# Kernel tuning notes

Measured on AMD Instinct MI355X. Metric: run time of the kernel, lower is better.

## Reference

```python
import jax, jax.numpy as jnp
import numpy as np

B, N, W, D = 32, 576, 32, 256  # batch, patches, max concepts per sample, embed dim


def _l2norm(x, eps=1e-12):
    # matches torch F.normalize: x / max(||x||, eps)
    n = jnp.linalg.norm(x, axis=-1, keepdims=True)
    return x / jnp.maximum(n, eps)


def setup_inputs() -> dict:
    key = jax.random.key(0)
    k1, k2, k3 = jax.random.split(key, 3)
    return {
        "image_token_features": jax.random.normal(k1, (B, N, D), dtype=jnp.float32),
        "concept_text_features": jax.random.normal(k2, (B, W, D), dtype=jnp.float32),
        "concept_lengths": jax.random.randint(k3, (B,), 1, W + 1, dtype=jnp.int32),
        "logit_scale": jnp.array([2.0], dtype=jnp.float32),   # log-scale, clamp(-10,10).exp()
        "logit_bias": jnp.array([-1.0], dtype=jnp.float32),
    }


def reference(image_token_features, concept_text_features, logit_scale, logit_bias, concept_lengths):
    img = _l2norm(image_token_features)          # (B, N, D)
    con = _l2norm(concept_text_features)         # (B, W, D)
    # A[m, c, n, w] = cos(patch_n of image m, concept_w of sample c)
    A = jnp.einsum('mnd,cwd->mcnw', img, con)    # (B, B, N, W) -- dominant intermediate
    max_per_concept = A.max(axis=2)              # max over patches -> (B, B, W)
    # masked mean over valid concepts (ragged lengths)
    mask = (jnp.arange(W)[None, :] < concept_lengths[:, None]).astype(img.dtype)  # (B, W)
    lens = concept_lengths.astype(img.dtype)     # all >= 1 by construction
    sim = jnp.sum(max_per_concept * mask[None, :, :], axis=-1) / lens[None, :]    # (B, B)
    t = jnp.exp(jnp.clip(logit_scale, -10.0, 10.0))[0]
    logits = jnp.clip(t * sim + logit_bias[0], -50.0, 50.0)
    z = 2.0 * jnp.eye(sim.shape[0], dtype=sim.dtype) - 1.0  # +1 diag, -1 off-diag
    loss = -jnp.mean(jax.nn.log_sigmoid(z * logits))
    return loss
```

## Files before the change

### kernel.cpp

```cpp
#include <hip/hip_runtime.h>
#include <hip/hip_bf16.h>
#include <math.h>

#define BB 32
#define NP 576
#define WW 32
#define DD 256

typedef __bf16 bf16x8 __attribute__((ext_vector_type(8)));
typedef float f32x4 __attribute__((ext_vector_type(4)));

__device__ __forceinline__ unsigned short f2bf(float f) {
  unsigned int u = __float_as_uint(f);
  u += 0x7FFFu + ((u >> 16) & 1u);
  return (unsigned short)(u >> 16);
}

__device__ __forceinline__ void gld_lds16(const unsigned short* g, unsigned short* l) {
  __builtin_amdgcn_global_load_lds(
      (const __attribute__((address_space(1))) void*)g,
      (__attribute__((address_space(3))) void*)l, 16, 0, 0);
}

__device__ __forceinline__ unsigned int encf(float f) {
  unsigned int b = __float_as_uint(f);
  return (b & 0x80000000u) ? ~b : (b | 0x80000000u);
}
__device__ __forceinline__ float decf(unsigned int u) {
  unsigned int b = (u & 0x80000000u) ? (u & 0x7FFFFFFFu) : ~u;
  return __uint_as_float(b);
}

__global__ __launch_bounds__(256) void norm_cast_kernel(
    const float* __restrict__ img, const float* __restrict__ con,
    unsigned short* __restrict__ img_t, unsigned short* __restrict__ con_t,
    unsigned int* __restrict__ sraw) {
  int gid = blockIdx.x * 256 + threadIdx.x;
  if (gid < BB * 1024) sraw[gid] = 0u;

  int row = blockIdx.x * 4 + (threadIdx.x >> 6);
  int lane = threadIdx.x & 63;
  const int n_img = BB * NP;
  const float* src;
  unsigned short* dstbase;
  int prow;
  if (row < n_img) {
    src = img + (size_t)row * DD;
    dstbase = img_t;
    prow = row;
  } else {
    prow = row - n_img;
    src = con + (size_t)prow * DD;
    dstbase = con_t;
  }
  float4 v = ((const float4*)src)[lane];
  float ss = v.x * v.x + v.y * v.y + v.z * v.z + v.w * v.w;
  #pragma unroll
  for (int off = 1; off < 64; off <<= 1) ss += __shfl_xor(ss, off);
  float inv = 1.0f / fmaxf(sqrtf(ss), 1e-12f);
  ushort4 o;
  o.x = f2bf(v.x * inv);
  o.y = f2bf(v.y * inv);
  o.z = f2bf(v.z * inv);
  o.w = f2bf(v.w * inv);
  size_t di = ((size_t)(prow >> 4) * 8 + (lane >> 3)) * 512 +
              (size_t)((((lane >> 1) & 3) * 16 + (prow & 15)) * 8) + (lane & 1) * 4;
  *(ushort4*)(dstbase + di) = o;
}

__global__ __launch_bounds__(256, 3) void gemm_max_kernel(
    const unsigned short* __restrict__ img_t,
    const unsigned short* __restrict__ con_t,
    unsigned int* __restrict__ sraw) {
  int bx = blockIdx.x;
  int bw = bx & 7;
  int bm = bx >> 3;
  int m = bm / 5;
  int t = bm - m * 5;
  int p0 = m * NP + t * 128;
  int w0 = bw * 128;

  __shared__ __align__(16) unsigned short ldsA[8192];
  __shared__ float sm[256];

  int tid = threadIdx.x;
  int wid = tid >> 6;
  int lane = tid & 63;
  int wp = wid >> 1;
  int wc = wid & 1;

  f32x4 acc[4][4];
  #pragma unroll
  for (int i = 0; i < 4; ++i)
    #pragma unroll
    for (int j = 0; j < 4; ++j) acc[i][j] = (f32x4){0.f, 0.f, 0.f, 0.f};

  const unsigned short* gA = img_t + (size_t)(p0 >> 4) * 4096 + lane * 8;
  const unsigned short* gB = con_t + ((size_t)(w0 >> 4) + wc * 4) * 4096 + lane * 8;

  for (int kb = 0; kb < 4; ++kb) {
    __syncthreads();
    #pragma unroll
    for (int u = 0; u < 4; ++u) {
      int s = wid * 4 + u;
      int gi = s >> 1;
      int kk2 = s & 1;
      gld_lds16(gA + ((size_t)gi * 8 + kb * 2 + kk2) * 512, &ldsA[s * 512]);
    }
    bf16x8 bfr[4][2];
    #pragma unroll
    for (int wj = 0; wj < 4; ++wj)
      #pragma unroll
      for (int kk = 0; kk < 2; ++kk)
        bfr[wj][kk] =
            *(const bf16x8*)(gB + ((size_t)wj * 8 + kb * 2 + kk) * 512);
    __syncthreads();
    #pragma unroll
    for (int kk = 0; kk < 2; ++kk) {
      bf16x8 af[4];
      #pragma unroll
      for (int pi = 0; pi < 4; ++pi)
        af[pi] = *(const bf16x8*)&ldsA[(((wp * 4 + pi) << 1) | kk) * 512 + lane * 8];
      #pragma unroll
      for (int pi = 0; pi < 4; ++pi)
        #pragma unroll
        for (int wj = 0; wj < 4; ++wj)
          acc[pi][wj] = __builtin_amdgcn_mfma_f32_16x16x32_bf16(
              af[pi], bfr[wj][kk], acc[pi][wj], 0, 0, 0);
    }
  }

  float mxw[4];
  #pragma unroll
  for (int wj = 0; wj < 4; ++wj) {
    float v = -1e30f;
    #pragma unroll
    for (int pi = 0; pi < 4; ++pi)
      v = fmaxf(v, fmaxf(fmaxf(acc[pi][wj][0], acc[pi][wj][1]),
                         fmaxf(acc[pi][wj][2], acc[pi][wj][3])));
    v = fmaxf(v, __shfl_xor(v, 16));
    v = fmaxf(v, __shfl_xor(v, 32));
    mxw[wj] = v;
  }
  __syncthreads();
  if (lane < 16) {
    #pragma unroll
    for (int wj = 0; wj < 4; ++wj)
      sm[wp * 128 + wc * 64 + wj * 16 + lane] = mxw[wj];
  }
  __syncthreads();
  if (tid < 128) {
    float v = sm[tid];
    if (t != 4) v = fmaxf(v, sm[128 + tid]);
    atomicMax(&sraw[(size_t)m * 1024 + w0 + tid], encf(v));
  }
}

__global__ __launch_bounds__(1024) void loss_kernel(
    const unsigned int* __restrict__ sraw, const int* __restrict__ lens,
    const float* __restrict__ lsc, const float* __restrict__ lbi,
    float* __restrict__ out) {
  int tid = threadIdx.x;
  int m = tid >> 5;
  int c = tid & 31;
  int len = lens[c];
  const unsigned int* base = sraw + (size_t)m * 1024 + c * 32;
  float s = 0.0f;
  for (int w = 0; w < WW; ++w)
    if (w < len) s += decf(base[w]);
  s /= (float)len;
  float tt = expf(fminf(fmaxf(lsc[0], -10.0f), 10.0f));
  float lg = fminf(fmaxf(tt * s + lbi[0], -50.0f), 50.0f);
  float x = (m == c) ? lg : -lg;
  float acc = (x >= 0.0f) ? -log1pf(expf(-x)) : (x - log1pf(expf(x)));
  #pragma unroll
  for (int off = 1; off < 64; off <<= 1) acc += __shfl_xor(acc, off);
  __shared__ float sred[16];
  if ((tid & 63) == 0) sred[tid >> 6] = acc;
  __syncthreads();
  if (tid == 0) {
    float tot = 0.0f;
    #pragma unroll
    for (int i = 0; i < 16; ++i) tot += sred[i];
    out[0] = -tot / (float)(BB * BB);
  }
}

extern "C" void kernel_launch(void* const* d_in, const int* in_sizes, int n_in,
                              void* d_out, int out_size, void* d_ws, size_t ws_size,
                              hipStream_t stream) {
  const float* img = (const float*)d_in[0];
  const float* con = (const float*)d_in[1];
  const int* lens = (const int*)d_in[2];
  const float* lsc = (const float*)d_in[3];
  const float* lbi = (const float*)d_in[4];

  unsigned short* img_t = (unsigned short*)d_ws;
  unsigned short* con_t = img_t + (size_t)BB * NP * DD;
  unsigned int* sraw = (unsigned int*)(con_t + (size_t)BB * WW * DD);

  norm_cast_kernel<<<(BB * NP + BB * WW) / 4, 256, 0, stream>>>(img, con, img_t,
                                                                con_t, sraw);
  gemm_max_kernel<<<160 * 8, 256, 0, stream>>>(img_t, con_t, sraw);
  loss_kernel<<<1, 1024, 0, stream>>>(sraw, lens, lsc, lbi, (float*)d_out);
}
```

Before: 102.5 us.

## Stage B tiles through LDS, coalesce norm-cast writes, remap blocks for XCD locality

The norm/cast kernel now handles 16 rows per 1024-thread block and stages the bf16 output in LDS. It then writes each 4096-element tile contiguously instead of scattering 8-byte stores. The GEMM kernel now loads concept (B) tiles into LDS with global_load_lds rather than per-wave direct global loads. Block indices are also remapped so that blocks sharing an image tile land on the same XCD for L2 reuse. The cost is extra LDS use in the GEMM, which may reduce occupancy, plus an extra barrier in the cast kernel.

```diff
diff --git a/kernel.cpp b/kernel.cpp
--- a/kernel.cpp
+++ b/kernel.cpp
@@ -31,29 +31,31 @@
   return __uint_as_float(b);
 }
 
-__global__ __launch_bounds__(256) void norm_cast_kernel(
+__global__ __launch_bounds__(1024) void norm_cast_kernel(
     const float* __restrict__ img, const float* __restrict__ con,
     unsigned short* __restrict__ img_t, unsigned short* __restrict__ con_t,
     unsigned int* __restrict__ sraw) {
-  int gid = blockIdx.x * 256 + threadIdx.x;
-  if (gid < BB * 1024) sraw[gid] = 0u;
-
-  int row = blockIdx.x * 4 + (threadIdx.x >> 6);
-  int lane = threadIdx.x & 63;
-  const int n_img = BB * NP;
+  __shared__ __align__(16) unsigned short lds[16 * 264];
+  int tid = threadIdx.x;
+  int g = blockIdx.x;
+  if (g < 32) sraw[g * 1024 + tid] = 0u;
+
+  int w = tid >> 6;
+  int L = tid & 63;
+  const int n_img_g = (BB * NP) >> 4;
   const float* src;
   unsigned short* dstbase;
-  int prow;
-  if (row < n_img) {
-    src = img + (size_t)row * DD;
+  int gl;
+  if (g < n_img_g) {
+    src = img + ((size_t)g * 16 + w) * DD;
     dstbase = img_t;
-    prow = row;
+    gl = g;
   } else {
-    prow = row - n_img;
-    src = con + (size_t)prow * DD;
+    gl = g - n_img_g;
+    src = con + ((size_t)gl * 16 + w) * DD;
     dstbase = con_t;
   }
-  float4 v = ((const float4*)src)[lane];
+  float4 v = ((const float4*)src)[L];
   float ss = v.x * v.x + v.y * v.y + v.z * v.z + v.w * v.w;
   #pragma unroll
   for (int off = 1; off < 64; off <<= 1) ss += __shfl_xor(ss, off);
@@ -63,9 +65,17 @@
   o.y = f2bf(v.y * inv);
   o.z = f2bf(v.z * inv);
   o.w = f2bf(v.w * inv);
-  size_t di = ((size_t)(prow >> 4) * 8 + (lane >> 3)) * 512 +
-              (size_t)((((lane >> 1) & 3) * 16 + (prow & 15)) * 8) + (lane & 1) * 4;
-  *(ushort4*)(dstbase + di) = o;
+  *(ushort4*)&lds[w * 264 + L * 4] = o;
+  __syncthreads();
+  int i = tid * 4;
+  int s = i >> 9;
+  int idx8 = (i & 511) >> 3;
+  int q = idx8 >> 4;
+  int r = idx8 & 15;
+  int ji = i & 7;
+  int k = (s >> 1) * 64 + (s & 1) * 32 + q * 8 + ji;
+  ushort4 val = *(const ushort4*)&lds[r * 264 + k];
+  *(ushort4*)(dstbase + (size_t)gl * 4096 + i) = val;
 }
 
 __global__ __launch_bounds__(256, 3) void gemm_max_kernel(
@@ -73,14 +83,17 @@
     const unsigned short* __restrict__ con_t,
     unsigned int* __restrict__ sraw) {
   int bx = blockIdx.x;
-  int bw = bx & 7;
-  int bm = bx >> 3;
+  int xcd = bx & 7;
+  int k2 = bx >> 3;
+  int bm = (k2 & ~7) | xcd;
+  int bw = k2 & 7;
   int m = bm / 5;
   int t = bm - m * 5;
   int p0 = m * NP + t * 128;
   int w0 = bw * 128;
 
   __shared__ __align__(16) unsigned short ldsA[8192];
+  __shared__ __align__(16) unsigned short ldsB[8192];
   __shared__ float sm[256];
 
   int tid = threadIdx.x;
@@ -96,7 +109,7 @@
     for (int j = 0; j < 4; ++j) acc[i][j] = (f32x4){0.f, 0.f, 0.f, 0.f};
 
   const unsigned short* gA = img_t + (size_t)(p0 >> 4) * 4096 + lane * 8;
-  const unsigned short* gB = con_t + ((size_t)(w0 >> 4) + wc * 4) * 4096 + lane * 8;
+  const unsigned short* gB = con_t + (size_t)(w0 >> 4) * 4096 + lane * 8;
 
   for (int kb = 0; kb < 4; ++kb) {
     __syncthreads();
@@ -105,28 +118,26 @@
       int s = wid * 4 + u;
       int gi = s >> 1;
       int kk2 = s & 1;
-      gld_lds16(gA + ((size_t)gi * 8 + kb * 2 + kk2) * 512, &ldsA[s * 512]);
+      size_t goff = ((size_t)gi * 8 + kb * 2 + kk2) * 512;
+      gld_lds16(gA + goff, &ldsA[s * 512]);
+      gld_lds16(gB + goff, &ldsB[s * 512]);
     }
-    bf16x8 bfr[4][2];
-    #pragma unroll
-    for (int wj = 0; wj < 4; ++wj)
-      #pragma unroll
-      for (int kk = 0; kk < 2; ++kk)
-        bfr[wj][kk] =
-            *(const bf16x8*)(gB + ((size_t)wj * 8 + kb * 2 + kk) * 512);
     __syncthreads();
     #pragma unroll
     for (int kk = 0; kk < 2; ++kk) {
-      bf16x8 af[4];
+      bf16x8 af[4], bfr[4];
       #pragma unroll
       for (int pi = 0; pi < 4; ++pi)
         af[pi] = *(const bf16x8*)&ldsA[(((wp * 4 + pi) << 1) | kk) * 512 + lane * 8];
       #pragma unroll
+      for (int wj = 0; wj < 4; ++wj)
+        bfr[wj] = *(const bf16x8*)&ldsB[(((wc * 4 + wj) << 1) | kk) * 512 + lane * 8];
+      #pragma unroll
       for (int pi = 0; pi < 4; ++pi)
         #pragma unroll
         for (int wj = 0; wj < 4; ++wj)
-          acc[pi][wj] = __builtin_amdgcn_mfma_f32_16x16x32_bf16(
-              af[pi], bfr[wj][kk], acc[pi][wj], 0, 0, 0);
+          acc[pi][wj] = __builtin_amdgcn_mfma_f32_16x16x32_bf16(af[pi], bfr[wj],
+                                                                acc[pi][wj], 0, 0, 0);
     }
   }
 
@@ -199,8 +210,7 @@
   unsigned short* con_t = img_t + (size_t)BB * NP * DD;
   unsigned int* sraw = (unsigned int*)(con_t + (size_t)BB * WW * DD);
 
-  norm_cast_kernel<<<(BB * NP + BB * WW) / 4, 256, 0, stream>>>(img, con, img_t,
-                                                                con_t, sraw);
+  norm_cast_kernel<<<1152 + 64, 1024, 0, stream>>>(img, con, img_t, con_t, sraw);
   gemm_max_kernel<<<160 * 8, 256, 0, stream>>>(img_t, con_t, sraw);
   loss_kernel<<<1, 1024, 0, stream>>>(sraw, lens, lsc, lbi, (float*)d_out);
 }
```

After: 97.74 us. -4.6%, faster.
